# Performance work log

Hardware: AMD Instinct MI355X
Metric: run time of the kernel (lower is better)

Reference implementation:

```python
import jax, jax.numpy as jnp
import numpy as np

C = 64      # hidden_channels (in == out)
H = 8       # heads
D = C // H  # per-head dim
NU = 100000 # users
NG = 50000  # games
E = 1000000 # edges per relation
NEG_SLOPE = 0.2


def setup_inputs() -> dict:
    key = jax.random.key(0)
    ks = jax.random.split(key, 24)
    p = lambda k, shp: (jax.random.normal(k, shp, dtype=jnp.float32) * 0.1)
    return {
        "x_user": jax.random.normal(ks[0], (NU, C), dtype=jnp.float32),
        "x_game": jax.random.normal(ks[1], (NG, C), dtype=jnp.float32),
        "plays_src": jax.random.randint(ks[2], (E,), 0, NU),
        "plays_dst": jax.random.randint(ks[3], (E,), 0, NG),
        "rec_src": jax.random.randint(ks[4], (E,), 0, NU),
        "rec_dst": jax.random.randint(ks[5], (E,), 0, NG),
        "W_user": p(ks[6], (C, C)), "b_user": p(ks[7], (C,)),
        "W_game": p(ks[8], (C, C)), "b_game": p(ks[9], (C,)),
        "att_src_pg": p(ks[10], (H, D)), "att_dst_pg": p(ks[11], (H, D)),
        "att_src_rg": p(ks[12], (H, D)), "att_dst_rg": p(ks[13], (H, D)),
        "att_src_pu": p(ks[14], (H, D)), "att_dst_pu": p(ks[15], (H, D)),
        "att_src_ru": p(ks[16], (H, D)), "att_dst_ru": p(ks[17], (H, D)),
        "k_lin_w": p(ks[18], (C, C)), "k_lin_b": p(ks[19], (C,)),
        "q": p(ks[20], (C,)),
    }


def _seg_softmax(alpha, seg, n):
    # PyG softmax: exp(a - segmax) / (segsum + 1e-16), grouped by dst node
    m = jax.ops.segment_max(alpha, seg, num_segments=n)  # [n, H]
    ex = jnp.exp(alpha - m[seg])
    s = jax.ops.segment_sum(ex, seg, num_segments=n)
    return ex / (s[seg] + 1e-16)


def _edge_agg(h_src, h_dst, a_s, a_d, src, dst, n_dst):
    # GAT-style per-edge-type attention; h_* are [N, H, D]
    al_s = (h_src * a_s).sum(-1)  # [N_src, H]
    al_d = (h_dst * a_d).sum(-1)  # [N_dst, H]
    alpha = al_s[src] + al_d[dst]  # [E, H]
    alpha = jnp.where(alpha >= 0, alpha, NEG_SLOPE * alpha)  # leaky_relu
    alpha = _seg_softmax(alpha, dst, n_dst)
    out = jax.ops.segment_sum(alpha[:, :, None] * h_src[src], dst,
                              num_segments=n_dst)  # [n_dst, H, D]
    return jax.nn.relu(out.reshape(n_dst, H * D))


def _semantic(outs, q, kw, kb):
    # semantic-level attention across metapaths
    stk = jnp.stack(outs)  # [M, N, C]
    score = (q * jnp.tanh(stk @ kw.T + kb).mean(axis=1)).sum(-1)  # [M]
    w = jax.nn.softmax(score)
    return (w[:, None, None] * stk).sum(0)  # [N, C]


def reference(x_user, x_game, plays_src, plays_dst, rec_src, rec_dst,
              W_user, b_user, W_game, b_game,
              att_src_pg, att_dst_pg, att_src_rg, att_dst_rg,
              att_src_pu, att_dst_pu, att_src_ru, att_dst_ru,
              k_lin_w, k_lin_b, q):
    h_u = (x_user @ W_user.T + b_user).reshape(NU, H, D)
    h_g = (x_game @ W_game.T + b_game).reshape(NG, H, D)
    # dst = game metapaths (user -> game)
    og_plays = _edge_agg(h_u, h_g, att_src_pg, att_dst_pg, plays_src, plays_dst, NG)
    og_rec = _edge_agg(h_u, h_g, att_src_rg, att_dst_rg, rec_src, rec_dst, NG)
    # dst = user metapaths (game -> user, reversed edges)
    ou_plays = _edge_agg(h_g, h_u, att_src_pu, att_dst_pu, plays_dst, plays_src, NU)
    ou_rec = _edge_agg(h_g, h_u, att_src_ru, att_dst_ru, rec_dst, rec_src, NU)
    out_user = _semantic([ou_plays, ou_rec], q, k_lin_w, k_lin_b)
    out_game = _semantic([og_plays, og_rec], q, k_lin_w, k_lin_b)
    return out_user, out_game
```

## Files before the change

### kernel.cpp

```cpp
#include <hip/hip_runtime.h>
#include <hip/hip_fp16.h>

#define NUSERS 100000
#define NGAMES 50000
#define NEDGES 1000000
#define NT     300000
#define NT4    75000
#define SCAN_B 293

struct KRel { const int* key; const int* payload; int base; unsigned short* rank; };
struct K4 { KRel r[4]; };
struct AggRel { const float* als; const float* ald; const __half* hsrc;
                float* outp; int base; int n_dst; };
struct ARels { AggRel r[4]; };
struct SemP { const float* p[4]; int n[4]; };
struct TParm { const float* x; const float* W; const float* b;
               const float* att0; const float* att1; const float* att2; const float* att3;
               __half* hout; float* al0; float* al1; float* al2; float* al3; int N; };
struct T2 { TParm t[2]; };

__global__ __launch_bounds__(256) void transform_kernel(T2 P) {
  TParm R = P.t[blockIdx.y];
  int nb = blockIdx.x*32;
  if (nb >= R.N) return;
  __shared__ float Wl[64][65];
  __shared__ float xl[4][64];
  int tid = threadIdx.x;
  for (int i = tid; i < 4096; i += 256) Wl[i>>6][i&63] = R.W[i];
  int nl = tid>>6, c = tid&63;
  float bc  = R.b[c];
  float a0c = R.att0[c], a1c = R.att1[c], a2c = R.att2[c], a3c = R.att3[c];
  for (int pass = 0; pass < 8; ++pass) {
    int n = nb + pass*4 + nl;
    __syncthreads();
    if (n < R.N) xl[nl][c] = R.x[(size_t)n*64 + c];
    __syncthreads();
    if (n >= R.N) continue;
    float acc = bc;
    #pragma unroll
    for (int k = 0; k < 64; ++k) acc += xl[nl][k]*Wl[c][k];
    R.hout[(size_t)n*64+c] = __float2half(acc);
    float p0 = acc*a0c, p1 = acc*a1c, p2 = acc*a2c, p3 = acc*a3c;
    #pragma unroll
    for (int mask = 1; mask < 8; mask <<= 1) {
      p0 += __shfl_xor(p0, mask);
      p1 += __shfl_xor(p1, mask);
      p2 += __shfl_xor(p2, mask);
      p3 += __shfl_xor(p3, mask);
    }
    int d = c&7, hh = c>>3;
    if      (d == 0) R.al0[n*8+hh] = p0;
    else if (d == 1) R.al1[n*8+hh] = p1;
    else if (d == 2) R.al2[n*8+hh] = p2;
    else if (d == 3) R.al3[n*8+hh] = p3;
  }
}

__global__ __launch_bounds__(256) void hist_rank_kernel(K4 P, int* __restrict__ deg) {
  KRel R = P.r[blockIdx.y];
  int e = blockIdx.x*256 + threadIdx.x;
  if (e >= NEDGES) return;
  R.rank[e] = (unsigned short)atomicAdd(&deg[R.base + R.key[e]], 1);
}

__global__ __launch_bounds__(256) void scan_blocksum(const int* __restrict__ deg,
                                                     int* __restrict__ bsum) {
  __shared__ int red[256];
  int t = threadIdx.x;
  int i4 = blockIdx.x*256 + t;
  int4 v = (i4 < NT4) ? ((const int4*)deg)[i4] : int4{0,0,0,0};
  red[t] = v.x+v.y+v.z+v.w;
  __syncthreads();
  for (int off = 128; off > 0; off >>= 1) {
    if (t < off) red[t] += red[t+off];
    __syncthreads();
  }
  if (t == 0) bsum[blockIdx.x] = red[0];
}

__global__ __launch_bounds__(512) void scan_top(const int* __restrict__ bsum,
                                                int* __restrict__ boff) {
  __shared__ int sc[512];
  int t = threadIdx.x;
  int v = (t < SCAN_B) ? bsum[t] : 0;
  sc[t] = v;
  __syncthreads();
  for (int off = 1; off < 512; off <<= 1) {
    int add = (t >= off) ? sc[t-off] : 0;
    __syncthreads();
    sc[t] += add;
    __syncthreads();
  }
  if (t < SCAN_B) boff[t] = sc[t] - v;
}

__global__ __launch_bounds__(256) void scan_final(const int* __restrict__ deg,
    const int* __restrict__ boff, int* __restrict__ start) {
  __shared__ int sc[256];
  int t = threadIdx.x;
  int i4 = blockIdx.x*256 + t;
  int4 v = (i4 < NT4) ? ((const int4*)deg)[i4] : int4{0,0,0,0};
  int s01 = v.x + v.y;
  int sum = s01 + v.z + v.w;
  sc[t] = sum;
  __syncthreads();
  for (int off = 1; off < 256; off <<= 1) {
    int add = (t >= off) ? sc[t-off] : 0;
    __syncthreads();
    sc[t] += add;
    __syncthreads();
  }
  int excl = sc[t] - sum + boff[blockIdx.x];
  if (i4 < NT4) {
    int4 st;
    st.x = excl;
    st.y = excl + v.x;
    st.z = excl + s01;
    st.w = excl + s01 + v.z;
    ((int4*)start)[i4] = st;
  }
}

__global__ __launch_bounds__(256) void scatter_kernel(K4 P,
    const int* __restrict__ start, int* __restrict__ src_sorted) {
  KRel R = P.r[blockIdx.y];
  int e = blockIdx.x*256 + threadIdx.x;
  if (e >= NEDGES) return;
  src_sorted[start[R.base + R.key[e]] + (int)R.rank[e]] = R.payload[e];
}

__global__ __launch_bounds__(256) void agg_kernel(ARels P,
    const int* __restrict__ csr_start, const int* __restrict__ deg,
    const int* __restrict__ src_sorted) {
  AggRel R = P.r[blockIdx.y];
  int lane = threadIdx.x & 63, wid = threadIdx.x >> 6;
  int n = blockIdx.x*4 + wid;
  if (n >= R.n_dst) return;
  int h = lane >> 3;
  float aldv = R.ald[(size_t)n*8 + h];
  int start = csr_start[R.base + n];
  int dcount = deg[R.base + n];
  float acc0 = 0.f, den0 = 0.f, acc1 = 0.f, den1 = 0.f;
  for (int j0 = 0; j0 < dcount; j0 += 64) {
    int idx = j0 + lane;
    int mysrc = (idx < dcount) ? src_sorted[start + idx] : 0;
    int cnt = dcount - j0; if (cnt > 64) cnt = 64;
    int jj = 0;
    for (; jj + 4 <= cnt; jj += 4) {
      int s0 = __shfl(mysrc, jj+0);
      int s1 = __shfl(mysrc, jj+1);
      int s2 = __shfl(mysrc, jj+2);
      int s3 = __shfl(mysrc, jj+3);
      float A0 = R.als[(size_t)s0*8 + h];
      float A1 = R.als[(size_t)s1*8 + h];
      float A2 = R.als[(size_t)s2*8 + h];
      float A3 = R.als[(size_t)s3*8 + h];
      float v0 = __half2float(R.hsrc[(size_t)s0*64 + lane]);
      float v1 = __half2float(R.hsrc[(size_t)s1*64 + lane]);
      float v2 = __half2float(R.hsrc[(size_t)s2*64 + lane]);
      float v3 = __half2float(R.hsrc[(size_t)s3*64 + lane]);
      A0 += aldv; A0 = A0 >= 0.f ? A0 : 0.2f*A0; float e0 = __expf(A0);
      A1 += aldv; A1 = A1 >= 0.f ? A1 : 0.2f*A1; float e1 = __expf(A1);
      A2 += aldv; A2 = A2 >= 0.f ? A2 : 0.2f*A2; float e2 = __expf(A2);
      A3 += aldv; A3 = A3 >= 0.f ? A3 : 0.2f*A3; float e3 = __expf(A3);
      den0 += e0 + e1; den1 += e2 + e3;
      acc0 = fmaf(e0, v0, acc0); acc1 = fmaf(e1, v1, acc1);
      acc0 = fmaf(e2, v2, acc0); acc1 = fmaf(e3, v3, acc1);
    }
    for (; jj < cnt; ++jj) {
      int s = __shfl(mysrc, jj);
      float a = R.als[(size_t)s*8 + h] + aldv;
      a = a >= 0.f ? a : 0.2f*a;
      float ex = __expf(a);
      den0 += ex;
      acc0 = fmaf(ex, __half2float(R.hsrc[(size_t)s*64 + lane]), acc0);
    }
  }
  float v = (acc0 + acc1) / (den0 + den1 + 1e-16f);
  R.outp[(size_t)n*64 + lane] = v > 0.f ? v : 0.f;
}

__global__ __launch_bounds__(256) void sem_stats_kernel(SemP P,
    const float* __restrict__ kw, const float* __restrict__ kb,
    float* __restrict__ semacc) {
  int mp = blockIdx.y;
  const float* O = P.p[mp]; int N = P.n[mp];
  __shared__ float Kl[64][65];
  __shared__ float xl[4][64];
  __shared__ float red[4][64];
  int tid = threadIdx.x;
  for (int i = tid; i < 4096; i += 256) Kl[i>>6][i&63] = kw[i];
  int nl = tid>>6, c = tid&63;
  float accsum = 0.f;
  for (int nb = blockIdx.x*4; nb < N; nb += gridDim.x*4) {
    __syncthreads();
    int node = nb + nl;
    xl[nl][c] = (node < N) ? O[(size_t)node*64+c] : 0.f;
    __syncthreads();
    if (node < N) {
      float y = kb[c];
      #pragma unroll
      for (int k = 0; k < 64; ++k) y += xl[nl][k]*Kl[c][k];
      accsum += tanhf(y);
    }
  }
  red[nl][c] = accsum;
  __syncthreads();
  if (tid < 64) {
    float tot = red[0][tid]+red[1][tid]+red[2][tid]+red[3][tid];
    atomicAdd(&semacc[mp*64+tid], tot);
  }
}

__global__ void sem_weights_kernel(const float* __restrict__ semacc,
                                   const float* __restrict__ q,
                                   float* __restrict__ w) {
  int c = threadIdx.x;
  float qc = q[c];
  float sc[4];
  const float invN[4] = {1.f/NUSERS, 1.f/NUSERS, 1.f/NGAMES, 1.f/NGAMES};
  #pragma unroll
  for (int m = 0; m < 4; ++m) {
    float v = qc * semacc[m*64+c] * invN[m];
    #pragma unroll
    for (int mask = 1; mask < 64; mask <<= 1) v += __shfl_xor(v, mask);
    sc[m] = v;
  }
  if (c == 0) {
    float m0 = fmaxf(sc[0], sc[1]);
    float e0 = expf(sc[0]-m0), e1 = expf(sc[1]-m0);
    w[0] = e0/(e0+e1); w[1] = e1/(e0+e1);
    float m1 = fmaxf(sc[2], sc[3]);
    float e2 = expf(sc[2]-m1), e3 = expf(sc[3]-m1);
    w[2] = e2/(e2+e3); w[3] = e3/(e2+e3);
  }
}

__global__ __launch_bounds__(256) void combine_kernel(
    float* __restrict__ out_u, const float* __restrict__ rec_u,
    float* __restrict__ out_g, const float* __restrict__ rec_g,
    const float* __restrict__ w) {
  int i = blockIdx.x*256 + threadIdx.x;
  if (blockIdx.y == 0) {
    if (i < NUSERS*64) out_u[i] = w[0]*out_u[i] + w[1]*rec_u[i];
  } else {
    if (i < NGAMES*64) out_g[i] = w[2]*out_g[i] + w[3]*rec_g[i];
  }
}

extern "C" void kernel_launch(void* const* d_in, const int* in_sizes, int n_in,
                              void* d_out_v, int out_size, void* d_ws, size_t ws_size,
                              hipStream_t stream) {
  const float* x_user     = (const float*)d_in[0];
  const float* x_game     = (const float*)d_in[1];
  const int*   plays_src  = (const int*)d_in[2];
  const int*   plays_dst  = (const int*)d_in[3];
  const int*   rec_src    = (const int*)d_in[4];
  const int*   rec_dst    = (const int*)d_in[5];
  const float* W_user     = (const float*)d_in[6];
  const float* b_user     = (const float*)d_in[7];
  const float* W_game     = (const float*)d_in[8];
  const float* b_game     = (const float*)d_in[9];
  const float* att_src_pg = (const float*)d_in[10];
  const float* att_dst_pg = (const float*)d_in[11];
  const float* att_src_rg = (const float*)d_in[12];
  const float* att_dst_rg = (const float*)d_in[13];
  const float* att_src_pu = (const float*)d_in[14];
  const float* att_dst_pu = (const float*)d_in[15];
  const float* att_src_ru = (const float*)d_in[16];
  const float* att_dst_ru = (const float*)d_in[17];
  const float* k_lin_w    = (const float*)d_in[18];
  const float* k_lin_b    = (const float*)d_in[19];
  const float* q          = (const float*)d_in[20];
  float* out = (float*)d_out_v;
  float* ws  = (float*)d_ws;

  size_t o = 0;
  __half* h_u16 = (__half*)(ws + o); o += (size_t)NUSERS*32;
  __half* h_g16 = (__half*)(ws + o); o += (size_t)NGAMES*32;
  float* alU0 = ws + o; o += (size_t)NUSERS*8;
  float* alU1 = ws + o; o += (size_t)NUSERS*8;
  float* alU2 = ws + o; o += (size_t)NUSERS*8;
  float* alU3 = ws + o; o += (size_t)NUSERS*8;
  float* alG0 = ws + o; o += (size_t)NGAMES*8;
  float* alG1 = ws + o; o += (size_t)NGAMES*8;
  float* alG2 = ws + o; o += (size_t)NGAMES*8;
  float* alG3 = ws + o; o += (size_t)NGAMES*8;
  float* acc1 = ws + o; o += (size_t)NGAMES*64;
  float* acc3 = ws + o; o += (size_t)NUSERS*64;
  float* semacc = ws + o; o += 256;
  float* wbuf   = ws + o; o += 4;
  int* deg        = (int*)(ws + o); o += NT;
  int* csr_start  = (int*)(ws + o); o += NT;
  int* bsum       = (int*)(ws + o); o += 512;
  int* boff       = (int*)(ws + o); o += 512;
  unsigned short* rank_all = (unsigned short*)(ws + o); o += (size_t)2*NEDGES;
  int* src_sorted = (int*)(ws + o); o += (size_t)4*NEDGES;

  float* out_u = out;
  float* out_g = out + (size_t)NUSERS*64;

  hipMemsetAsync(deg, 0, (size_t)NT*sizeof(int), stream);
  hipMemsetAsync(semacc, 0, 260*sizeof(float), stream);

  T2 TP;
  TP.t[0] = {x_user, W_user, b_user, att_src_pg, att_src_rg, att_dst_pu, att_dst_ru,
             h_u16, alU0, alU1, alU2, alU3, NUSERS};
  TP.t[1] = {x_game, W_game, b_game, att_dst_pg, att_dst_rg, att_src_pu, att_src_ru,
             h_g16, alG0, alG1, alG2, alG3, NGAMES};
  transform_kernel<<<dim3((NUSERS+31)/32, 2), 256, 0, stream>>>(TP);

  K4 KP;
  KP.r[0] = {plays_dst, plays_src, 0,               rank_all + 0*(size_t)NEDGES};
  KP.r[1] = {rec_dst,   rec_src,   NGAMES,          rank_all + 1*(size_t)NEDGES};
  KP.r[2] = {plays_src, plays_dst, 2*NGAMES,        rank_all + 2*(size_t)NEDGES};
  KP.r[3] = {rec_src,   rec_dst,   2*NGAMES+NUSERS, rank_all + 3*(size_t)NEDGES};

  hist_rank_kernel<<<dim3((NEDGES+255)/256, 4), 256, 0, stream>>>(KP, deg);
  scan_blocksum<<<dim3(SCAN_B), 256, 0, stream>>>(deg, bsum);
  scan_top<<<dim3(1), 512, 0, stream>>>(bsum, boff);
  scan_final<<<dim3(SCAN_B), 256, 0, stream>>>(deg, boff, csr_start);
  scatter_kernel<<<dim3((NEDGES+255)/256, 4), 256, 0, stream>>>(KP, csr_start, src_sorted);

  ARels AP;
  AP.r[0] = {alU0, alG0, h_u16, out_g, 0,                 NGAMES};
  AP.r[1] = {alU1, alG1, h_u16, acc1,  NGAMES,            NGAMES};
  AP.r[2] = {alG2, alU2, h_g16, out_u, 2*NGAMES,          NUSERS};
  AP.r[3] = {alG3, alU3, h_g16, acc3,  2*NGAMES+NUSERS,   NUSERS};

  agg_kernel<<<dim3((NUSERS+3)/4, 4), 256, 0, stream>>>(AP, csr_start, deg, src_sorted);

  SemP S;
  S.p[0] = out_u; S.p[1] = acc3; S.p[2] = out_g; S.p[3] = acc1;
  S.n[0] = NUSERS; S.n[1] = NUSERS; S.n[2] = NGAMES; S.n[3] = NGAMES;
  sem_stats_kernel<<<dim3(256,4), 256, 0, stream>>>(S, k_lin_w, k_lin_b, semacc);
  sem_weights_kernel<<<1, 64, 0, stream>>>(semacc, q, wbuf);
  combine_kernel<<<dim3((NUSERS*64+255)/256, 2), 256, 0, stream>>>(out_u, acc3, out_g, acc1, wbuf);
}
```

Before: 764.6 us.

## Fuse transform with degree histogram and register-tile semantic stats kernel

Merges the node transform and edge-degree histogram kernels into one launch, dispatching on block index so the compute-bound GEMV blocks and the atomic-bound histogram blocks can overlap. The semantic stats kernel now stages 32 nodes per block and gives each thread 8 nodes so each weight read from shared memory is reused. It also replaces tanhf with an exp-based formula. The grid for that kernel is doubled. The risks are lower occupancy from the larger shared buffer and a small loss of tanh accuracy.

```diff
diff --git a/kernel.cpp b/kernel.cpp
--- a/kernel.cpp
+++ b/kernel.cpp
@@ -7,6 +7,9 @@
 #define NT     300000
 #define NT4    75000
 #define SCAN_B 293
+#define TUB    3125
+#define TGB    1563
+#define HB     3907
 
 struct KRel { const int* key; const int* payload; int base; unsigned short* rank; };
 struct K4 { KRel r[4]; };
@@ -19,48 +22,53 @@
                __half* hout; float* al0; float* al1; float* al2; float* al3; int N; };
 struct T2 { TParm t[2]; };
 
-__global__ __launch_bounds__(256) void transform_kernel(T2 P) {
-  TParm R = P.t[blockIdx.y];
-  int nb = blockIdx.x*32;
-  if (nb >= R.N) return;
-  __shared__ float Wl[64][65];
-  __shared__ float xl[4][64];
-  int tid = threadIdx.x;
-  for (int i = tid; i < 4096; i += 256) Wl[i>>6][i&63] = R.W[i];
-  int nl = tid>>6, c = tid&63;
-  float bc  = R.b[c];
-  float a0c = R.att0[c], a1c = R.att1[c], a2c = R.att2[c], a3c = R.att3[c];
-  for (int pass = 0; pass < 8; ++pass) {
-    int n = nb + pass*4 + nl;
-    __syncthreads();
-    if (n < R.N) xl[nl][c] = R.x[(size_t)n*64 + c];
-    __syncthreads();
-    if (n >= R.N) continue;
-    float acc = bc;
-    #pragma unroll
-    for (int k = 0; k < 64; ++k) acc += xl[nl][k]*Wl[c][k];
-    R.hout[(size_t)n*64+c] = __float2half(acc);
-    float p0 = acc*a0c, p1 = acc*a1c, p2 = acc*a2c, p3 = acc*a3c;
-    #pragma unroll
-    for (int mask = 1; mask < 8; mask <<= 1) {
-      p0 += __shfl_xor(p0, mask);
-      p1 += __shfl_xor(p1, mask);
-      p2 += __shfl_xor(p2, mask);
-      p3 += __shfl_xor(p3, mask);
-    }
-    int d = c&7, hh = c>>3;
-    if      (d == 0) R.al0[n*8+hh] = p0;
-    else if (d == 1) R.al1[n*8+hh] = p1;
-    else if (d == 2) R.al2[n*8+hh] = p2;
-    else if (d == 3) R.al3[n*8+hh] = p3;
-  }
-}
-
-__global__ __launch_bounds__(256) void hist_rank_kernel(K4 P, int* __restrict__ deg) {
-  KRel R = P.r[blockIdx.y];
-  int e = blockIdx.x*256 + threadIdx.x;
-  if (e >= NEDGES) return;
-  R.rank[e] = (unsigned short)atomicAdd(&deg[R.base + R.key[e]], 1);
+__global__ __launch_bounds__(256) void trans_hist_kernel(T2 TP, K4 KP,
+                                                         int* __restrict__ deg) {
+  int bid = blockIdx.x;
+  if (bid < TUB + TGB) {
+    TParm R = (bid < TUB) ? TP.t[0] : TP.t[1];
+    int nb = (bid < TUB ? bid : bid - TUB) * 32;
+    if (nb >= R.N) return;
+    __shared__ float Wl[64][65];
+    __shared__ float xl[4][64];
+    int tid = threadIdx.x;
+    for (int i = tid; i < 4096; i += 256) Wl[i>>6][i&63] = R.W[i];
+    int nl = tid>>6, c = tid&63;
+    float bc  = R.b[c];
+    float a0c = R.att0[c], a1c = R.att1[c], a2c = R.att2[c], a3c = R.att3[c];
+    for (int pass = 0; pass < 8; ++pass) {
+      int n = nb + pass*4 + nl;
+      __syncthreads();
+      if (n < R.N) xl[nl][c] = R.x[(size_t)n*64 + c];
+      __syncthreads();
+      if (n >= R.N) continue;
+      float acc = bc;
+      #pragma unroll
+      for (int k = 0; k < 64; ++k) acc += xl[nl][k]*Wl[c][k];
+      R.hout[(size_t)n*64+c] = __float2half(acc);
+      float p0 = acc*a0c, p1 = acc*a1c, p2 = acc*a2c, p3 = acc*a3c;
+      #pragma unroll
+      for (int mask = 1; mask < 8; mask <<= 1) {
+        p0 += __shfl_xor(p0, mask);
+        p1 += __shfl_xor(p1, mask);
+        p2 += __shfl_xor(p2, mask);
+        p3 += __shfl_xor(p3, mask);
+      }
+      int d = c&7, hh = c>>3;
+      if      (d == 0) R.al0[n*8+hh] = p0;
+      else if (d == 1) R.al1[n*8+hh] = p1;
+      else if (d == 2) R.al2[n*8+hh] = p2;
+      else if (d == 3) R.al3[n*8+hh] = p3;
+    }
+  } else {
+    int hb  = bid - (TUB + TGB);
+    int rel = hb / HB;
+    int eb  = hb - rel*HB;
+    KRel R = KP.r[rel];
+    int e = eb*256 + threadIdx.x;
+    if (e >= NEDGES) return;
+    R.rank[e] = (unsigned short)atomicAdd(&deg[R.base + R.key[e]], 1);
+  }
 }
 
 __global__ __launch_bounds__(256) void scan_blocksum(const int* __restrict__ deg,
@@ -186,25 +194,40 @@
   int mp = blockIdx.y;
   const float* O = P.p[mp]; int N = P.n[mp];
   __shared__ float Kl[64][65];
-  __shared__ float xl[4][64];
+  __shared__ float xl[32][64];
   __shared__ float red[4][64];
   int tid = threadIdx.x;
   for (int i = tid; i < 4096; i += 256) Kl[i>>6][i&63] = kw[i];
-  int nl = tid>>6, c = tid&63;
+  int g = tid>>6, c = tid&63;
+  float kbc = kb[c];
   float accsum = 0.f;
-  for (int nb = blockIdx.x*4; nb < N; nb += gridDim.x*4) {
-    __syncthreads();
-    int node = nb + nl;
-    xl[nl][c] = (node < N) ? O[(size_t)node*64+c] : 0.f;
-    __syncthreads();
-    if (node < N) {
-      float y = kb[c];
+  for (int nb = blockIdx.x*32; nb < N; nb += gridDim.x*32) {
+    __syncthreads();
+    #pragma unroll
+    for (int t = 0; t < 8; ++t) {
+      int i = tid + t*256;
+      int node = nb + (i>>6);
+      xl[i>>6][i&63] = (node < N) ? O[(size_t)node*64 + (i&63)] : 0.f;
+    }
+    __syncthreads();
+    float acc[8] = {0.f,0.f,0.f,0.f,0.f,0.f,0.f,0.f};
+    #pragma unroll
+    for (int k = 0; k < 64; ++k) {
+      float Kc = Kl[c][k];
       #pragma unroll
-      for (int k = 0; k < 64; ++k) y += xl[nl][k]*Kl[c][k];
-      accsum += tanhf(y);
-    }
-  }
-  red[nl][c] = accsum;
+      for (int j = 0; j < 8; ++j)
+        acc[j] = fmaf(xl[g*8+j][k], Kc, acc[j]);
+    }
+    int rem = N - nb - g*8;
+    #pragma unroll
+    for (int j = 0; j < 8; ++j) {
+      if (j < rem) {
+        float e2 = __expf(2.f*(acc[j] + kbc));
+        accsum += 1.f - 2.f/(e2 + 1.f);
+      }
+    }
+  }
+  red[g][c] = accsum;
   __syncthreads();
   if (tid < 64) {
     float tot = red[0][tid]+red[1][tid]+red[2][tid]+red[3][tid];
@@ -308,7 +331,6 @@
              h_u16, alU0, alU1, alU2, alU3, NUSERS};
   TP.t[1] = {x_game, W_game, b_game, att_dst_pg, att_dst_rg, att_src_pu, att_src_ru,
              h_g16, alG0, alG1, alG2, alG3, NGAMES};
-  transform_kernel<<<dim3((NUSERS+31)/32, 2), 256, 0, stream>>>(TP);
 
   K4 KP;
   KP.r[0] = {plays_dst, plays_src, 0,               rank_all + 0*(size_t)NEDGES};
@@ -316,7 +338,7 @@
   KP.r[2] = {plays_src, plays_dst, 2*NGAMES,        rank_all + 2*(size_t)NEDGES};
   KP.r[3] = {rec_src,   rec_dst,   2*NGAMES+NUSERS, rank_all + 3*(size_t)NEDGES};
 
-  hist_rank_kernel<<<dim3((NEDGES+255)/256, 4), 256, 0, stream>>>(KP, deg);
+  trans_hist_kernel<<<dim3(TUB + TGB + 4*HB), 256, 0, stream>>>(TP, KP, deg);
   scan_blocksum<<<dim3(SCAN_B), 256, 0, stream>>>(deg, bsum);
   scan_top<<<dim3(1), 512, 0, stream>>>(bsum, boff);
   scan_final<<<dim3(SCAN_B), 256, 0, stream>>>(deg, boff, csr_start);
@@ -333,7 +355,7 @@
   SemP S;
   S.p[0] = out_u; S.p[1] = acc3; S.p[2] = out_g; S.p[3] = acc1;
   S.n[0] = NUSERS; S.n[1] = NUSERS; S.n[2] = NGAMES; S.n[3] = NGAMES;
-  sem_stats_kernel<<<dim3(256,4), 256, 0, stream>>>(S, k_lin_w, k_lin_b, semacc);
+  sem_stats_kernel<<<dim3(512,4), 256, 0, stream>>>(S, k_lin_w, k_lin_b, semacc);
   sem_weights_kernel<<<1, 64, 0, stream>>>(semacc, q, wbuf);
   combine_kernel<<<dim3((NUSERS*64+255)/256, 2), 256, 0, stream>>>(out_u, acc3, out_g, acc1, wbuf);
 }
```

Result: slower. 944.1 us (+23.5%).
